# Optimization experiments

Hardware: AMD Instinct MI355X
Metric: run time of the kernel (lower is better)

The kernel has to match this reference:

```python
import jax, jax.numpy as jnp
import numpy as np

B, H, T, D, R = 2, 12, 2048, 64, 16
D_STD = D - R


def setup_inputs() -> dict:
    key = jax.random.key(0)
    ks = jax.random.split(key, 5)
    return {
        "Q": jax.random.normal(ks[0], (B, H, T, D), jnp.float32),
        "K": jax.random.normal(ks[1], (B, H, T, D), jnp.float32),
        "V": jax.random.normal(ks[2], (B, H, T, D), jnp.float32),
        "d_bias": jax.random.normal(ks[3], (B, H, T), jnp.float32),
        "W_recip": jax.random.normal(ks[4], (D, R), jnp.float32) * 0.02,
        "w_std": jnp.full((H,), 0.5, jnp.float32),
        "w_rec": jnp.full((H,), 0.3, jnp.float32),
        "w_disc": jnp.full((H,), 0.2, jnp.float32),
    }


def reference(Q, K, V, d_bias, W_recip, w_std, w_rec, w_disc):
    b, h, t, d = Q.shape
    r = W_recip.shape[1]
    d_std = d - r
    sq_std = jnp.sqrt(w_std)[None, :, None, None]  # [1,H,1,1]
    sq_rec = jnp.sqrt(w_rec)[None, :, None, None]
    Q_low = jnp.einsum("bhtd,dr->bhtr", Q, W_recip)  # [B,H,T,R]
    K_low = jnp.einsum("bhtd,dr->bhtr", K, W_recip)
    Q_aug = jnp.concatenate([sq_std * Q[..., :d_std], sq_rec * K_low], axis=-1)  # [B,H,T,D]
    K_aug = jnp.concatenate([sq_std * K[..., :d_std], sq_rec * Q_low], axis=-1)
    scale = 1.0 / jnp.sqrt(jnp.asarray(d, Q.dtype))
    scores = jnp.einsum("bhqd,bhkd->bhqk", Q_aug, K_aug) * scale  # [B,H,T,T]
    # rank-1 additive bias, broadcast over queries: bias[b,h,q,k] = w_disc[h]*d_bias[b,h,k]
    scores = scores + (w_disc[None, :, None, None] * d_bias[:, :, None, :])
    causal = jnp.tril(jnp.ones((t, t), bool))  # [T,T]
    scores = jnp.where(causal[None, None], scores, -jnp.inf)
    attn = jax.nn.softmax(scores, axis=-1)
    return jnp.einsum("bhqk,bhkd->bhqd", attn, V)
```

## Files before the change

kernel.cpp:

```cpp
#include <hip/hip_runtime.h>
#include <math.h>

#define T_SEQ 2048
#define NH    12
#define NB    2
#define BHC   (NB*NH)
#define NQT   32

typedef _Float16 half4_t __attribute__((ext_vector_type(4)));
typedef _Float16 half8_t __attribute__((ext_vector_type(8)));
typedef float    floatx4 __attribute__((ext_vector_type(4)));

__device__ __forceinline__ half8_t h8splat(_Float16 s) {
  return (half8_t){s, s, s, s, s, s, s, s};
}

__global__ __launch_bounds__(256) void prep_kernel(
    const float* __restrict__ Q, const float* __restrict__ K,
    const float* __restrict__ V, const float* __restrict__ W,
    const float* __restrict__ wstd, const float* __restrict__ wrec,
    const float* __restrict__ dbias, const float* __restrict__ wdisc,
    ushort* __restrict__ QF, ushort* __restrict__ KF, ushort* __restrict__ VF,
    float* __restrict__ B2)
{
  __shared__ __align__(16) _Float16 Qsh[64*72];
  __shared__ __align__(16) _Float16 Ksh[64*72];
  __shared__ __align__(16) _Float16 Vsh[64*72];
  __shared__ __align__(16) _Float16 Lqh[64*16];
  __shared__ __align__(16) _Float16 Lkh[64*16];

  const int tid = threadIdx.x;
  const int w = tid >> 6, lane = tid & 63;
  const int quad = lane >> 4, ln = lane & 15;
  const int bh = blockIdx.x >> 5, tblk = blockIdx.x & 31;
  const long g0 = ((long)bh * T_SEQ + tblk * 64) * 64;

  const float4* gQ = (const float4*)(Q + g0);
  const float4* gK = (const float4*)(K + g0);
  const float4* gV = (const float4*)(V + g0);
  for (int i = tid; i < 1024; i += 256) {
    int r = i >> 4, c4 = i & 15;
    float4 q = gQ[i], k = gK[i], v = gV[i];
    *(half4_t*)&Qsh[r*72 + c4*4] = (half4_t){(_Float16)q.x,(_Float16)q.y,(_Float16)q.z,(_Float16)q.w};
    *(half4_t*)&Ksh[r*72 + c4*4] = (half4_t){(_Float16)k.x,(_Float16)k.y,(_Float16)k.z,(_Float16)k.w};
    *(half4_t*)&Vsh[r*72 + c4*4] = (half4_t){(_Float16)v.x,(_Float16)v.y,(_Float16)v.z,(_Float16)v.w};
  }
  __syncthreads();

  half4_t bw[4];
#pragma unroll
  for (int dk = 0; dk < 4; dk++)
#pragma unroll
    for (int i = 0; i < 4; i++)
      bw[dk][i] = (_Float16)W[(dk*16 + quad*4 + i)*16 + ln];

  floatx4 cq = {0.f,0.f,0.f,0.f}, ck = {0.f,0.f,0.f,0.f};
#pragma unroll
  for (int dk = 0; dk < 4; dk++) {
    half4_t aq = *(const half4_t*)&Qsh[(w*16 + ln)*72 + dk*16 + quad*4];
    half4_t ak = *(const half4_t*)&Ksh[(w*16 + ln)*72 + dk*16 + quad*4];
    cq = __builtin_amdgcn_mfma_f32_16x16x16f16(aq, bw[dk], cq, 0, 0, 0);
    ck = __builtin_amdgcn_mfma_f32_16x16x16f16(ak, bw[dk], ck, 0, 0, 0);
  }
#pragma unroll
  for (int i = 0; i < 4; i++) {
    Lqh[(w*16 + quad*4 + i)*16 + ln] = (_Float16)cq[i];
    Lkh[(w*16 + quad*4 + i)*16 + ln] = (_Float16)ck[i];
  }
  __syncthreads();

  const int h = bh % NH;
  const float LOG2E = 1.4426950408889634f;
  const float sstd = sqrtf(wstd[h]);
  const float srec = sqrtf(wrec[h]);
  const half8_t hq_std = h8splat((_Float16)(0.125f * sstd * LOG2E));
  const half8_t hk_std = h8splat((_Float16)sstd);
  const half8_t hq_rec = h8splat((_Float16)(0.125f * srec * LOG2E));
  const half8_t hk_rec = h8splat((_Float16)srec);

  if (tid < 64) B2[(long)bh*T_SEQ + tblk*64 + tid] =
      LOG2E * wdisc[h] * dbias[(long)bh*T_SEQ + tblk*64 + tid];

#pragma unroll
  for (int cc = 0; cc < 2; cc++) {
    int c = tid + cc * 256;
    {
      int lp = c & 63, dp = (c >> 6) & 1, rt = c >> 7;
      int row = rt*16 + (lp & 15);
      int d0 = dp*32 + (lp >> 4)*8;
      half8_t hq, hk;
      if (d0 < 48) {
        hq = *(const half8_t*)&Qsh[row*72 + d0] * hq_std;
        hk = *(const half8_t*)&Ksh[row*72 + d0] * hk_std;
      } else {
        hq = *(const half8_t*)&Lkh[row*16 + (d0-48)] * hq_rec;
        hk = *(const half8_t*)&Lqh[row*16 + (d0-48)] * hk_rec;
      }
      long tile16 = (long)bh*128 + tblk*4 + rt;
      ((int4*)QF)[tile16*128 + dp*64 + lp] = *(int4*)&hq;
      ((int4*)KF)[tile16*128 + dp*64 + lp] = *(int4*)&hk;
    }
    {
      int lv = c & 63, nt = (c >> 6) & 3, v2 = c >> 8;
      int d = nt*16 + (lv & 15), qv = lv >> 4;
      half8_t hv;
#pragma unroll
      for (int j = 0; j < 4; j++) {
        hv[j]   = Vsh[(v2*32 + qv*4 + j)*72 + d];
        hv[4+j] = Vsh[(v2*32 + 16 + qv*4 + j)*72 + d];
      }
      ((int4*)VF)[((long)bh*32 + tblk)*512 + (v2*4 + nt)*64 + lv] = *(int4*)&hv;
    }
  }
}

__global__ __launch_bounds__(128, 3) void flash_kernel(
    const ushort* __restrict__ QF, const ushort* __restrict__ KF,
    const ushort* __restrict__ VF, const float* __restrict__ B2,
    float* __restrict__ Out)
{
  __shared__ float sm1[16];
  __shared__ float sl1[16];
  __shared__ float sacc1[64*16];

  const int tid  = threadIdx.x;
  const int wv   = tid >> 6;
  const int lane = tid & 63;
  const int quad = lane >> 4, ln = lane & 15;
  const int bid = blockIdx.x;
  const int bh  = bid % BHC;
  const int t16 = 127 - bid / BHC;
  const int qrow = t16*16 + ln;
  const int ktmax = t16 >> 2;

  const ushort* gK = KF + (long)bh * 131072;
  const ushort* gV = VF + (long)bh * 131072;
  const float*  gB = B2 + (long)bh * T_SEQ;

  half8_t bq[2];
  {
    const ushort* gQ = QF + ((long)bh*128 + t16) * 1024;
    bq[0] = *(const half8_t*)(gQ + lane*8);
    bq[1] = *(const half8_t*)(gQ + 512 + lane*8);
  }

  float m_i = -1e30f, l_i = 0.f;
  floatx4 acc[4];
#pragma unroll
  for (int nt = 0; nt < 4; nt++) acc[nt] = (floatx4){0.f,0.f,0.f,0.f};

  const int kt0 = wv;
  const long oo0 = (long)(kt0 <= ktmax ? kt0 : 0) * 4096;
  half8_t kf[8], vf[8];
#pragma unroll
  for (int c = 0; c < 8; c++) {
    kf[c] = *(const half8_t*)(gK + oo0 + c*512 + lane*8);
    vf[c] = *(const half8_t*)(gV + oo0 + c*512 + lane*8);
  }

  for (int kt = kt0; kt <= ktmax; kt += 2) {
    const long onx = (long)(kt + 2 <= ktmax ? kt + 2 : kt) * 4096;

    floatx4 st[4];
#pragma unroll
    for (int mt = 0; mt < 4; mt++) {
      floatx4 c = (floatx4){0.f,0.f,0.f,0.f};
      c = __builtin_amdgcn_mfma_f32_16x16x32_f16(kf[mt*2],     bq[0], c, 0, 0, 0);
      c = __builtin_amdgcn_mfma_f32_16x16x32_f16(kf[mt*2 + 1], bq[1], c, 0, 0, 0);
      st[mt] = c;
    }
#pragma unroll
    for (int c = 0; c < 8; c++)
      kf[c] = *(const half8_t*)(gK + onx + c*512 + lane*8);

    const bool diag = (kt == ktmax);
    float rowmax = -1e30f;
#pragma unroll
    for (int mt = 0; mt < 4; mt++) {
      float4 bb = *(const float4*)(gB + kt*64 + mt*16 + quad*4);
      float bv[4] = {bb.x, bb.y, bb.z, bb.w};
#pragma unroll
      for (int i = 0; i < 4; i++) {
        float v = st[mt][i] + bv[i];
        int key = kt*64 + mt*16 + quad*4 + i;
        if (diag && key > qrow) v = -1e30f;
        st[mt][i] = v;
        rowmax = fmaxf(rowmax, v);
      }
    }
    rowmax = fmaxf(rowmax, __shfl_xor(rowmax, 16));
    rowmax = fmaxf(rowmax, __shfl_xor(rowmax, 32));

    if (!__all(rowmax <= m_i + 8.f)) {
      float mnew  = fmaxf(m_i, rowmax);
      float alpha = exp2f(m_i - mnew);
      float af[4];
#pragma unroll
      for (int i = 0; i < 4; i++) af[i] = __shfl(alpha, quad*4 + i);
#pragma unroll
      for (int nt = 0; nt < 4; nt++)
#pragma unroll
        for (int i = 0; i < 4; i++) acc[nt][i] *= af[i];
      l_i *= alpha;
      m_i  = mnew;
    }

    float psum = 0.f;
    half4_t pa[4];
#pragma unroll
    for (int mt = 0; mt < 4; mt++)
#pragma unroll
      for (int i = 0; i < 4; i++) {
        float p = exp2f(st[mt][i] - m_i);
        psum += p;
        pa[mt][i] = (_Float16)p;
      }
    psum += __shfl_xor(psum, 16);
    psum += __shfl_xor(psum, 32);
    l_i += psum;

#pragma unroll
    for (int v2 = 0; v2 < 2; v2++)
#pragma unroll
      for (int nt = 0; nt < 4; nt++) {
        half8_t vv = vf[v2*4 + nt];
        half4_t b0 = __builtin_shufflevector(vv, vv, 0,1,2,3);
        half4_t b1 = __builtin_shufflevector(vv, vv, 4,5,6,7);
        acc[nt] = __builtin_amdgcn_mfma_f32_16x16x16f16(pa[2*v2],   b0, acc[nt], 0, 0, 0);
        acc[nt] = __builtin_amdgcn_mfma_f32_16x16x16f16(pa[2*v2+1], b1, acc[nt], 0, 0, 0);
      }
#pragma unroll
    for (int c = 0; c < 8; c++)
      vf[c] = *(const half8_t*)(gV + onx + c*512 + lane*8);
  }

  if (wv == 1) {
    if (quad == 0) { sm1[ln] = m_i; sl1[ln] = l_i; }
#pragma unroll
    for (int nt = 0; nt < 4; nt++)
#pragma unroll
      for (int i = 0; i < 4; i++)
        sacc1[lane*16 + nt*4 + i] = acc[nt][i];
  }
  __syncthreads();
  if (wv == 0) {
    const float m1  = sm1[ln];
    const float l1v = sl1[ln];
    const float mm  = fmaxf(m_i, m1);
    const float w0  = exp2f(m_i - mm);
    const float w1  = exp2f(m1  - mm);
    const float lm  = l_i * w0 + l1v * w1;
    float w0r[4], w1r[4], lr[4];
#pragma unroll
    for (int i = 0; i < 4; i++) {
      w0r[i] = __shfl(w0, quad*4 + i);
      w1r[i] = __shfl(w1, quad*4 + i);
      lr[i]  = 1.f / __shfl(lm, quad*4 + i);
    }
    const long obase = (long)bh*T_SEQ*64 + (long)(t16*16)*64;
#pragma unroll
    for (int i = 0; i < 4; i++)
#pragma unroll
      for (int nt = 0; nt < 4; nt++) {
        float4 a1 = *(const float4*)&sacc1[lane*16 + nt*4];
        Out[obase + (quad*4 + i)*64 + nt*16 + ln] =
            (acc[nt][i]*w0r[i] + ((const float*)&a1)[i]*w1r[i]) * lr[i];
      }
  }
}

extern "C" void kernel_launch(void* const* d_in, const int* in_sizes, int n_in,
                              void* d_out, int out_size, void* d_ws, size_t ws_size,
                              hipStream_t stream) {
  const float* Q     = (const float*)d_in[0];
  const float* K     = (const float*)d_in[1];
  const float* V     = (const float*)d_in[2];
  const float* dbias = (const float*)d_in[3];
  const float* W     = (const float*)d_in[4];
  const float* wstd  = (const float*)d_in[5];
  const float* wrec  = (const float*)d_in[6];
  const float* wdisc = (const float*)d_in[7];
  float* Out = (float*)d_out;

  const long NEL = (long)BHC * T_SEQ * 64;
  ushort* QF = (ushort*)d_ws;
  ushort* KF = QF + NEL;
  ushort* VF = KF + NEL;
  float*  B2 = (float*)(VF + NEL);

  prep_kernel<<<BHC * NQT, 256, 0, stream>>>(Q, K, V, W, wstd, wrec, dbias, wdisc,
                                             QF, KF, VF, B2);
  flash_kernel<<<BHC * 128, 128, 0, stream>>>(QF, KF, VF, B2, Out);
}
```

Before: 130.7 us.

## Process two 16-row query tiles per block to reuse K/V fragments

Each flash block now handles two adjacent 16-row query tiles (32 rows), keeping two sets of softmax state and accumulators while sharing the K and V fragments and bias loads loaded per key tile. The grid is halved. This halves K/V global loads per query row and doubles MFMA work per load. The cost is more registers per thread, which may reduce occupancy under launch_bounds(128,3), and fewer blocks for load balancing across the causal triangle.

Result: slower. 179.0 us (+37.0%).

```diff
diff --git a/kernel.cpp b/kernel.cpp
--- a/kernel.cpp
+++ b/kernel.cpp
@@ -119,9 +119,9 @@
     const ushort* __restrict__ VF, const float* __restrict__ B2,
     float* __restrict__ Out)
 {
-  __shared__ float sm1[16];
-  __shared__ float sl1[16];
-  __shared__ float sacc1[64*16];
+  __shared__ float sm1[2][16];
+  __shared__ float sl1[2][16];
+  __shared__ float sacc1[2][64*16];
 
   const int tid  = threadIdx.x;
   const int wv   = tid >> 6;
@@ -129,25 +129,32 @@
   const int quad = lane >> 4, ln = lane & 15;
   const int bid = blockIdx.x;
   const int bh  = bid % BHC;
-  const int t16 = 127 - bid / BHC;
-  const int qrow = t16*16 + ln;
-  const int ktmax = t16 >> 2;
+  const int p   = 63 - bid / BHC;
+  const int t16a = 2*p;
+  const int qa = t16a*16 + ln;
+  const int qb = qa + 16;
+  const int ktmax = p >> 1;
 
   const ushort* gK = KF + (long)bh * 131072;
   const ushort* gV = VF + (long)bh * 131072;
   const float*  gB = B2 + (long)bh * T_SEQ;
 
-  half8_t bq[2];
+  half8_t bqa[2], bqb[2];
   {
-    const ushort* gQ = QF + ((long)bh*128 + t16) * 1024;
-    bq[0] = *(const half8_t*)(gQ + lane*8);
-    bq[1] = *(const half8_t*)(gQ + 512 + lane*8);
-  }
-
-  float m_i = -1e30f, l_i = 0.f;
-  floatx4 acc[4];
-#pragma unroll
-  for (int nt = 0; nt < 4; nt++) acc[nt] = (floatx4){0.f,0.f,0.f,0.f};
+    const ushort* gQ = QF + ((long)bh*128 + t16a) * 1024;
+    bqa[0] = *(const half8_t*)(gQ + lane*8);
+    bqa[1] = *(const half8_t*)(gQ + 512 + lane*8);
+    bqb[0] = *(const half8_t*)(gQ + 1024 + lane*8);
+    bqb[1] = *(const half8_t*)(gQ + 1536 + lane*8);
+  }
+
+  float mA = -1e30f, lA = 0.f, mB = -1e30f, lB = 0.f;
+  floatx4 accA[4], accB[4];
+#pragma unroll
+  for (int nt = 0; nt < 4; nt++) {
+    accA[nt] = (floatx4){0.f,0.f,0.f,0.f};
+    accB[nt] = (floatx4){0.f,0.f,0.f,0.f};
+  }
 
   const int kt0 = wv;
   const long oo0 = (long)(kt0 <= ktmax ? kt0 : 0) * 4096;
@@ -161,63 +168,111 @@
   for (int kt = kt0; kt <= ktmax; kt += 2) {
     const long onx = (long)(kt + 2 <= ktmax ? kt + 2 : kt) * 4096;
 
-    floatx4 st[4];
+    float4 bb[4];
+#pragma unroll
+    for (int mt = 0; mt < 4; mt++)
+      bb[mt] = *(const float4*)(gB + kt*64 + mt*16 + quad*4);
+
+    floatx4 sta[4], stb[4];
 #pragma unroll
     for (int mt = 0; mt < 4; mt++) {
-      floatx4 c = (floatx4){0.f,0.f,0.f,0.f};
-      c = __builtin_amdgcn_mfma_f32_16x16x32_f16(kf[mt*2],     bq[0], c, 0, 0, 0);
-      c = __builtin_amdgcn_mfma_f32_16x16x32_f16(kf[mt*2 + 1], bq[1], c, 0, 0, 0);
-      st[mt] = c;
+      floatx4 ca = (floatx4){0.f,0.f,0.f,0.f};
+      ca = __builtin_amdgcn_mfma_f32_16x16x32_f16(kf[mt*2],     bqa[0], ca, 0, 0, 0);
+      ca = __builtin_amdgcn_mfma_f32_16x16x32_f16(kf[mt*2 + 1], bqa[1], ca, 0, 0, 0);
+      sta[mt] = ca;
+      floatx4 cb = (floatx4){0.f,0.f,0.f,0.f};
+      cb = __builtin_amdgcn_mfma_f32_16x16x32_f16(kf[mt*2],     bqb[0], cb, 0, 0, 0);
+      cb = __builtin_amdgcn_mfma_f32_16x16x32_f16(kf[mt*2 + 1], bqb[1], cb, 0, 0, 0);
+      stb[mt] = cb;
     }
 #pragma unroll
     for (int c = 0; c < 8; c++)
       kf[c] = *(const half8_t*)(gK + onx + c*512 + lane*8);
 
     const bool diag = (kt == ktmax);
-    float rowmax = -1e30f;
-#pragma unroll
-    for (int mt = 0; mt < 4; mt++) {
-      float4 bb = *(const float4*)(gB + kt*64 + mt*16 + quad*4);
-      float bv[4] = {bb.x, bb.y, bb.z, bb.w};
-#pragma unroll
-      for (int i = 0; i < 4; i++) {
-        float v = st[mt][i] + bv[i];
-        int key = kt*64 + mt*16 + quad*4 + i;
-        if (diag && key > qrow) v = -1e30f;
-        st[mt][i] = v;
-        rowmax = fmaxf(rowmax, v);
-      }
-    }
-    rowmax = fmaxf(rowmax, __shfl_xor(rowmax, 16));
-    rowmax = fmaxf(rowmax, __shfl_xor(rowmax, 32));
-
-    if (!__all(rowmax <= m_i + 8.f)) {
-      float mnew  = fmaxf(m_i, rowmax);
-      float alpha = exp2f(m_i - mnew);
-      float af[4];
-#pragma unroll
-      for (int i = 0; i < 4; i++) af[i] = __shfl(alpha, quad*4 + i);
-#pragma unroll
-      for (int nt = 0; nt < 4; nt++)
-#pragma unroll
-        for (int i = 0; i < 4; i++) acc[nt][i] *= af[i];
-      l_i *= alpha;
-      m_i  = mnew;
-    }
-
-    float psum = 0.f;
-    half4_t pa[4];
-#pragma unroll
-    for (int mt = 0; mt < 4; mt++)
-#pragma unroll
-      for (int i = 0; i < 4; i++) {
-        float p = exp2f(st[mt][i] - m_i);
-        psum += p;
-        pa[mt][i] = (_Float16)p;
-      }
-    psum += __shfl_xor(psum, 16);
-    psum += __shfl_xor(psum, 32);
-    l_i += psum;
+
+    half4_t paA[4], paB[4];
+    {
+      float rowmax = -1e30f;
+#pragma unroll
+      for (int mt = 0; mt < 4; mt++)
+#pragma unroll
+        for (int i = 0; i < 4; i++) {
+          float v = sta[mt][i] + ((const float*)&bb[mt])[i];
+          int key = kt*64 + mt*16 + quad*4 + i;
+          if (diag && key > qa) v = -1e30f;
+          sta[mt][i] = v;
+          rowmax = fmaxf(rowmax, v);
+        }
+      rowmax = fmaxf(rowmax, __shfl_xor(rowmax, 16));
+      rowmax = fmaxf(rowmax, __shfl_xor(rowmax, 32));
+      if (!__all(rowmax <= mA + 8.f)) {
+        float mnew  = fmaxf(mA, rowmax);
+        float alpha = exp2f(mA - mnew);
+        float af[4];
+#pragma unroll
+        for (int i = 0; i < 4; i++) af[i] = __shfl(alpha, quad*4 + i);
+#pragma unroll
+        for (int nt = 0; nt < 4; nt++)
+#pragma unroll
+          for (int i = 0; i < 4; i++) accA[nt][i] *= af[i];
+        lA *= alpha;
+        mA  = mnew;
+      }
+      float psum = 0.f;
+#pragma unroll
+      for (int mt = 0; mt < 4; mt++)
+#pragma unroll
+        for (int i = 0; i < 4; i++) {
+          float pv = exp2f(sta[mt][i] - mA);
+          psum += pv;
+          paA[mt][i] = (_Float16)pv;
+        }
+      psum += __shfl_xor(psum, 16);
+      psum += __shfl_xor(psum, 32);
+      lA += psum;
+    }
+
+    {
+      float rowmax = -1e30f;
+#pragma unroll
+      for (int mt = 0; mt < 4; mt++)
+#pragma unroll
+        for (int i = 0; i < 4; i++) {
+          float v = stb[mt][i] + ((const float*)&bb[mt])[i];
+          int key = kt*64 + mt*16 + quad*4 + i;
+          if (diag && key > qb) v = -1e30f;
+          stb[mt][i] = v;
+          rowmax = fmaxf(rowmax, v);
+        }
+      rowmax = fmaxf(rowmax, __shfl_xor(rowmax, 16));
+      rowmax = fmaxf(rowmax, __shfl_xor(rowmax, 32));
+      if (!__all(rowmax <= mB + 8.f)) {
+        float mnew  = fmaxf(mB, rowmax);
+        float alpha = exp2f(mB - mnew);
+        float af[4];
+#pragma unroll
+        for (int i = 0; i < 4; i++) af[i] = __shfl(alpha, quad*4 + i);
+#pragma unroll
+        for (int nt = 0; nt < 4; nt++)
+#pragma unroll
+          for (int i = 0; i < 4; i++) accB[nt][i] *= af[i];
+        lB *= alpha;
+        mB  = mnew;
+      }
+      float psum = 0.f;
+#pragma unroll
+      for (int mt = 0; mt < 4; mt++)
+#pragma unroll
+        for (int i = 0; i < 4; i++) {
+          float pv = exp2f(stb[mt][i] - mB);
+          psum += pv;
+          paB[mt][i] = (_Float16)pv;
+        }
+      psum += __shfl_xor(psum, 16);
+      psum += __shfl_xor(psum, 32);
+      lB += psum;
+    }
 
 #pragma unroll
     for (int v2 = 0; v2 < 2; v2++)
@@ -226,8 +281,10 @@
         half8_t vv = vf[v2*4 + nt];
         half4_t b0 = __builtin_shufflevector(vv, vv, 0,1,2,3);
         half4_t b1 = __builtin_shufflevector(vv, vv, 4,5,6,7);
-        acc[nt] = __builtin_amdgcn_mfma_f32_16x16x16f16(pa[2*v2],   b0, acc[nt], 0, 0, 0);
-        acc[nt] = __builtin_amdgcn_mfma_f32_16x16x16f16(pa[2*v2+1], b1, acc[nt], 0, 0, 0);
+        accA[nt] = __builtin_amdgcn_mfma_f32_16x16x16f16(paA[2*v2],   b0, accA[nt], 0, 0, 0);
+        accA[nt] = __builtin_amdgcn_mfma_f32_16x16x16f16(paA[2*v2+1], b1, accA[nt], 0, 0, 0);
+        accB[nt] = __builtin_amdgcn_mfma_f32_16x16x16f16(paB[2*v2],   b0, accB[nt], 0, 0, 0);
+        accB[nt] = __builtin_amdgcn_mfma_f32_16x16x16f16(paB[2*v2+1], b1, accB[nt], 0, 0, 0);
       }
 #pragma unroll
     for (int c = 0; c < 8; c++)
@@ -235,37 +292,48 @@
   }
 
   if (wv == 1) {
-    if (quad == 0) { sm1[ln] = m_i; sl1[ln] = l_i; }
+    if (quad == 0) {
+      sm1[0][ln] = mA; sl1[0][ln] = lA;
+      sm1[1][ln] = mB; sl1[1][ln] = lB;
+    }
 #pragma unroll
     for (int nt = 0; nt < 4; nt++)
 #pragma unroll
-      for (int i = 0; i < 4; i++)
-        sacc1[lane*16 + nt*4 + i] = acc[nt][i];
+      for (int i = 0; i < 4; i++) {
+        sacc1[0][lane*16 + nt*4 + i] = accA[nt][i];
+        sacc1[1][lane*16 + nt*4 + i] = accB[nt][i];
+      }
   }
   __syncthreads();
   if (wv == 0) {
-    const float m1  = sm1[ln];
-    const float l1v = sl1[ln];
-    const float mm  = fmaxf(m_i, m1);
-    const float w0  = exp2f(m_i - mm);
-    const float w1  = exp2f(m1  - mm);
-    const float lm  = l_i * w0 + l1v * w1;
-    float w0r[4], w1r[4], lr[4];
-#pragma unroll
-    for (int i = 0; i < 4; i++) {
-      w0r[i] = __shfl(w0, quad*4 + i);
-      w1r[i] = __shfl(w1, quad*4 + i);
-      lr[i]  = 1.f / __shfl(lm, quad*4 + i);
-    }
-    const long obase = (long)bh*T_SEQ*64 + (long)(t16*16)*64;
-#pragma unroll
-    for (int i = 0; i < 4; i++)
-#pragma unroll
-      for (int nt = 0; nt < 4; nt++) {
-        float4 a1 = *(const float4*)&sacc1[lane*16 + nt*4];
-        Out[obase + (quad*4 + i)*64 + nt*16 + ln] =
-            (acc[nt][i]*w0r[i] + ((const float*)&a1)[i]*w1r[i]) * lr[i];
-      }
+#pragma unroll
+    for (int t = 0; t < 2; t++) {
+      const float m0v = (t == 0) ? mA : mB;
+      const float l0v = (t == 0) ? lA : lB;
+      const floatx4* acc0 = (t == 0) ? accA : accB;
+      const float m1v = sm1[t][ln];
+      const float l1v = sl1[t][ln];
+      const float mm  = fmaxf(m0v, m1v);
+      const float w0  = exp2f(m0v - mm);
+      const float w1  = exp2f(m1v - mm);
+      const float lm  = l0v * w0 + l1v * w1;
+      float w0r[4], w1r[4], lr[4];
+#pragma unroll
+      for (int i = 0; i < 4; i++) {
+        w0r[i] = __shfl(w0, quad*4 + i);
+        w1r[i] = __shfl(w1, quad*4 + i);
+        lr[i]  = 1.f / __shfl(lm, quad*4 + i);
+      }
+      const long obase = (long)bh*T_SEQ*64 + (long)((t16a + t)*16)*64;
+#pragma unroll
+      for (int i = 0; i < 4; i++)
+#pragma unroll
+        for (int nt = 0; nt < 4; nt++) {
+          float4 a1 = *(const float4*)&sacc1[t][lane*16 + nt*4];
+          Out[obase + (quad*4 + i)*64 + nt*16 + ln] =
+              (acc0[nt][i]*w0r[i] + ((const float*)&a1)[i]*w1r[i]) * lr[i];
+        }
+    }
   }
 }
 
@@ -290,5 +358,5 @@
 
   prep_kernel<<<BHC * NQT, 256, 0, stream>>>(Q, K, V, W, wstd, wrec, dbias, wdisc,
                                              QF, KF, VF, B2);
-  flash_kernel<<<BHC * 128, 128, 0, stream>>>(QF, KF, VF, B2, Out);
+  flash_kernel<<<BHC * 64, 128, 0, stream>>>(QF, KF, VF, B2, Out);
 }
```
